# Kernel optimization log

Measured on AMD Instinct MI355X. Metric: run time of the kernel, lower is better.

## Reference

```python
import jax, jax.numpy as jnp
import numpy as np

N_NODES = 50000
N_EDGES = 600000
FEAT = 128
HID = 256


def _sage_gcn(feats, src, dst, W, b, n_nodes):
    # DGL SAGEConv aggregator_type='gcn':
    # h_neigh = (sum_{u in N(v)} h_u + h_v) / (in_deg(v) + 1); out = h_neigh @ W + b
    neigh_sum = jax.ops.segment_sum(feats[src], dst, num_segments=n_nodes)  # [N, d]
    in_deg = jax.ops.segment_sum(jnp.ones((src.shape[0],), feats.dtype), dst,
                                 num_segments=n_nodes)  # [N]
    h = (neigh_sum + feats) / (in_deg + 1.0)[:, None]
    return h @ W + b


def setup_inputs() -> dict:
    key = jax.random.key(0)
    ks = jax.random.split(key, 8)
    s = lambda d: 1.0 / np.sqrt(d)
    return {
        "features": jax.random.normal(ks[0], (N_NODES, FEAT), jnp.float32),
        "src": jax.random.randint(ks[1], (N_EDGES,), 0, N_NODES, jnp.int32),
        "dst": jax.random.randint(ks[2], (N_EDGES,), 0, N_NODES, jnp.int32),
        "W1": jax.random.normal(ks[3], (FEAT, HID), jnp.float32) * s(FEAT),
        "b1": jnp.zeros((HID,), jnp.float32),
        "W2": jax.random.normal(ks[4], (HID, HID), jnp.float32) * s(HID),
        "b2": jnp.zeros((HID,), jnp.float32),
        "Wd1": jax.random.normal(ks[5], (HID, HID), jnp.float32) * s(HID),
        "bd1": jnp.zeros((HID,), jnp.float32),
        "Wd2": jax.random.normal(ks[6], (HID, 1), jnp.float32) * s(HID),
        "bd2": jnp.zeros((1,), jnp.float32),
    }


def reference(features, src, dst, W1, b1, W2, b2, Wd1, bd1, Wd2, bd2):
    n = features.shape[0]
    # Encoder: SAGEConv(gcn) -> ReLU -> SAGEConv(gcn)   (dropout inactive in eval)
    h = _sage_gcn(features, src, dst, W1, b1, n)
    h = jax.nn.relu(h)
    h = _sage_gcn(h, src, dst, W2, b2, n)
    # Decoder: Linear -> ReLU -> Linear
    h = jax.nn.relu(h @ Wd1 + bd1)
    return h @ Wd2 + bd2  # [N, 1]
```

## Files before the change

### kernel.cpp

```cpp
#include <hip/hip_runtime.h>
#include <type_traits>

#define NN 50000
#define NE 600000
#define FEAT 128
#define HID 256
#define MAXD 64

typedef float v4f __attribute__((ext_vector_type(4)));
typedef float f32x4 __attribute__((ext_vector_type(4)));
typedef __bf16 bf16x8 __attribute__((ext_vector_type(8)));
using u16 = unsigned short;
using u32 = unsigned int;
typedef u16 u16x4 __attribute__((ext_vector_type(4)));
typedef u16 u16x8 __attribute__((ext_vector_type(8)));

__device__ __forceinline__ u16 f2bf(float f) {
    u32 u = __builtin_bit_cast(u32, f);
    u += 0x7fffu + ((u >> 16) & 1u);
    return (u16)(u >> 16);
}
__device__ __forceinline__ float bf2f(u16 h) {
    u32 u = ((u32)h) << 16;
    return __builtin_bit_cast(float, u);
}

#define NB_FILL 2344
#define NB_CVT 6250
#define NB_W1  128
#define NB_W2  256
#define NB_WD1 256
__global__ __launch_bounds__(256) void prep_fill_k(const int* __restrict__ src,
                                                   const int* __restrict__ dst,
                                                   int* __restrict__ cnt,
                                                   int* __restrict__ ell,
                                                   const float* __restrict__ feats,
                                                   const float* __restrict__ W1,
                                                   const float* __restrict__ W2,
                                                   const float* __restrict__ Wd1,
                                                   u16* __restrict__ featsbf,
                                                   u16* __restrict__ WT1,
                                                   u16* __restrict__ WT2,
                                                   u16* __restrict__ WTd1) {
    int b = blockIdx.x, t = threadIdx.x;
    if (b < NB_FILL) {
        int e = b * 256 + t;
        if (e < NE) {
            int d = dst[e];
            int p = atomicAdd(&cnt[d], 1);
            if (p < MAXD) ell[(size_t)d * MAXD + p] = src[e];
        }
        return;
    }
    b -= NB_FILL;
    if (b < NB_CVT) {
        int i = b * 256 + t;
        v4f v = *(const v4f*)(feats + (size_t)i * 4);
        u16x4 o;
        #pragma unroll
        for (int j = 0; j < 4; j++) o[j] = f2bf(v[j]);
        *(u16x4*)(featsbf + (size_t)i * 4) = o;
    } else if (b < NB_CVT + NB_W1) {
        int idx = (b - NB_CVT) * 256 + t;
        int k = idx >> 8, n = idx & 255;
        WT1[(size_t)n * 128 + k] = f2bf(W1[idx]);
    } else if (b < NB_CVT + NB_W1 + NB_W2) {
        int idx = (b - NB_CVT - NB_W1) * 256 + t;
        int k = idx >> 8, n = idx & 255;
        WT2[(size_t)n * 256 + k] = f2bf(W2[idx]);
    } else {
        int idx = (b - NB_CVT - NB_W1 - NB_W2) * 256 + t;
        int k = idx >> 8, n = idx & 255;
        WTd1[(size_t)n * 256 + k] = f2bf(Wd1[idx]);
    }
}

template <int D>
__global__ __launch_bounds__(256) void aggregate_bf_k(const u16* __restrict__ x,
                                                      const int* __restrict__ cnt,
                                                      const int* __restrict__ ell,
                                                      u16* __restrict__ o) {
    constexpr int LPG = (D == 256) ? 32 : 16;
    constexpr int G = 64 / LPG;
    int wave = threadIdx.x >> 6;
    int lane = threadIdx.x & 63;
    int v = blockIdx.x * 4 + wave;
    if (v >= NN) return;
    int g  = lane / LPG;
    int li = lane & (LPG - 1);
    size_t coff = (size_t)li * 8;
    int deg = cnt[v]; if (deg > MAXD) deg = MAXD;
    int cntv = deg + 1;
    const int* cols = ell + (size_t)v * MAXD;
    float acc[8];
    #pragma unroll
    for (int i = 0; i < 8; i++) acc[i] = 0.f;
    int base = 0;
    #pragma unroll 4
    for (; base + G <= cntv; base += G) {
        int idx = base + g;
        int row = (idx < deg) ? cols[idx] : v;
        u16x8 r = *(const u16x8*)(x + (size_t)row * D + coff);
        #pragma unroll
        for (int i = 0; i < 8; i++) acc[i] += bf2f(r[i]);
    }
    if (base + g < cntv) {
        int idx = base + g;
        int row = (idx < deg) ? cols[idx] : v;
        u16x8 r = *(const u16x8*)(x + (size_t)row * D + coff);
        #pragma unroll
        for (int i = 0; i < 8; i++) acc[i] += bf2f(r[i]);
    }
    #pragma unroll
    for (int i = 0; i < 8; i++) {
        acc[i] += __shfl_xor(acc[i], 32, 64);
        if (G == 4) acc[i] += __shfl_xor(acc[i], 16, 64);
    }
    if (lane < LPG) {
        float inv = 1.0f / (float)cntv;
        u16x8 O;
        #pragma unroll
        for (int i = 0; i < 8; i++) O[i] = f2bf(acc[i] * inv);
        *(u16x8*)(o + (size_t)v * D + coff) = O;
    }
}

__global__ __launch_bounds__(256) void agg2_dec_k(const u16* __restrict__ x,
                                                  const int* __restrict__ cnt,
                                                  const int* __restrict__ ell,
                                                  const float* __restrict__ bd1,
                                                  const float* __restrict__ wd2,
                                                  const float* __restrict__ bd2,
                                                  float* __restrict__ out) {
    int wave = threadIdx.x >> 6;
    int lane = threadIdx.x & 63;
    int v = blockIdx.x * 4 + wave;
    if (v >= NN) return;
    int g  = lane >> 5;
    int li = lane & 31;
    size_t coff = (size_t)li * 8;
    int deg = cnt[v]; if (deg > MAXD) deg = MAXD;
    int cntv = deg + 1;
    const int* cols = ell + (size_t)v * MAXD;
    float acc[8];
    #pragma unroll
    for (int i = 0; i < 8; i++) acc[i] = 0.f;
    int base = 0;
    #pragma unroll 4
    for (; base + 2 <= cntv; base += 2) {
        int idx = base + g;
        int row = (idx < deg) ? cols[idx] : v;
        u16x8 r = *(const u16x8*)(x + (size_t)row * 256 + coff);
        #pragma unroll
        for (int i = 0; i < 8; i++) acc[i] += bf2f(r[i]);
    }
    if (base + g < cntv) {
        int idx = base + g;
        int row = (idx < deg) ? cols[idx] : v;
        u16x8 r = *(const u16x8*)(x + (size_t)row * 256 + coff);
        #pragma unroll
        for (int i = 0; i < 8; i++) acc[i] += bf2f(r[i]);
    }
    #pragma unroll
    for (int i = 0; i < 8; i++) acc[i] += __shfl_xor(acc[i], 32, 64);

    float inv = 1.0f / (float)cntv;
    v4f b0 = *(const v4f*)(bd1 + li * 8);
    v4f b1 = *(const v4f*)(bd1 + li * 8 + 4);
    v4f w0 = *(const v4f*)(wd2 + li * 8);
    v4f w1 = *(const v4f*)(wd2 + li * 8 + 4);
    float p = 0.f;
    #pragma unroll
    for (int i = 0; i < 4; i++) p += fmaxf(acc[i] * inv + b0[i], 0.f) * w0[i];
    #pragma unroll
    for (int i = 0; i < 4; i++) p += fmaxf(acc[i + 4] * inv + b1[i], 0.f) * w1[i];
    p += __shfl_xor(p, 1, 64);
    p += __shfl_xor(p, 2, 64);
    p += __shfl_xor(p, 4, 64);
    p += __shfl_xor(p, 8, 64);
    p += __shfl_xor(p, 16, 64);
    if (lane == 0) out[v] = p + bd2[0];
}

#define MFMA_BF16 __builtin_amdgcn_mfma_f32_16x16x32_bf16
#define SW(s, r) (((s) ^ (((r) >> 1) & 3)) * 8)

#define MFMA_STEP(pa0, pa1, pa2, pa3, ph0, ph1)              \
    do {                                                     \
        acc[0][0] = MFMA_BF16(pa0, ph0, acc[0][0], 0, 0, 0); \
        acc[0][1] = MFMA_BF16(pa0, ph1, acc[0][1], 0, 0, 0); \
        acc[1][0] = MFMA_BF16(pa1, ph0, acc[1][0], 0, 0, 0); \
        acc[1][1] = MFMA_BF16(pa1, ph1, acc[1][1], 0, 0, 0); \
        acc[2][0] = MFMA_BF16(pa2, ph0, acc[2][0], 0, 0, 0); \
        acc[2][1] = MFMA_BF16(pa2, ph1, acc[2][1], 0, 0, 0); \
        acc[3][0] = MFMA_BF16(pa3, ph0, acc[3][0], 0, 0, 0); \
        acc[3][1] = MFMA_BF16(pa3, ph1, acc[3][1], 0, 0, 0); \
    } while (0)

__global__ __launch_bounds__(512, 4) void fused_gemm123_k(const u16* __restrict__ A1,
                                                          const u16* __restrict__ B1,
                                                          const float* __restrict__ b1,
                                                          const u16* __restrict__ B2,
                                                          const float* __restrict__ b2,
                                                          const u16* __restrict__ B3,
                                                          u16* __restrict__ Z, int M) {
    __shared__ __attribute__((aligned(16))) u16 sA[2][64 * 32];
    __shared__ __attribute__((aligned(16))) u16 sB[2][256 * 32];
    __shared__ __attribute__((aligned(16))) u16 sH[64 * 264];

    int tid = threadIdx.x;
    int wid = tid >> 6, lane = tid & 63;
    int m0 = blockIdx.x * 64;
    int r16 = lane & 15, sl = lane >> 4, k8 = sl * 8;

    u32 ao[4], bo[2];
    #pragma unroll
    for (int mf = 0; mf < 4; mf++) {
        int ar = mf * 16 + r16;
        ao[mf] = ar * 32 + SW(sl, ar);
    }
    #pragma unroll
    for (int nf = 0; nf < 2; nf++) {
        int bc = wid * 32 + nf * 16 + r16;
        bo[nf] = bc * 32 + SW(sl, bc);
    }

    f32x4 acc[4][2];
    #pragma unroll
    for (int a = 0; a < 4; a++)
        #pragma unroll
        for (int b = 0; b < 2; b++) acc[a][b] = (f32x4)0.f;

    int aRow = tid >> 2, aS = tid & 3;
    u32 aSw = aRow * 32 + SW(aS, aRow);
    int gAr = m0 + aRow; if (gAr >= M) gAr = M - 1;
    const u16* gA = A1 + (size_t)gAr * 128 + aS * 8;
    int bRow[2], bS[2]; u32 bSw[2];
    #pragma unroll
    for (int j = 0; j < 2; j++) {
        int idx = tid + j * 512;
        bRow[j] = idx >> 2; bS[j] = idx & 3;
        bSw[j] = bRow[j] * 32 + SW(bS[j], bRow[j]);
    }

    uint4 rA, rB0, rB1;

    if (tid < 256) rA = *(const uint4*)gA;
    rB0 = *(const uint4*)(B1 + (size_t)bRow[0] * 128 + bS[0] * 8);
    rB1 = *(const uint4*)(B1 + (size_t)bRow[1] * 128 + bS[1] * 8);
    if (tid < 256) *(uint4*)(&sA[0][aSw]) = rA;
    *(uint4*)(&sB[0][bSw[0]]) = rB0;
    *(uint4*)(&sB[0][bSw[1]]) = rB1;
    __syncthreads();

    #pragma unroll
    for (int kb = 0; kb < 4; kb++) {
        int cur = kb & 1;
        if (kb < 3) {
            if (tid < 256) rA = *(const uint4*)(gA + (kb + 1) * 32);
            rB0 = *(const uint4*)(B1 + (size_t)bRow[0] * 128 + (kb + 1) * 32 + bS[0] * 8);
            rB1 = *(const uint4*)(B1 + (size_t)bRow[1] * 128 + (kb + 1) * 32 + bS[1] * 8);
        }
        bf16x8 a0 = *(const bf16x8*)(&sA[cur][ao[0]]);
        bf16x8 a1 = *(const bf16x8*)(&sA[cur][ao[1]]);
        bf16x8 a2 = *(const bf16x8*)(&sA[cur][ao[2]]);
        bf16x8 a3 = *(const bf16x8*)(&sA[cur][ao[3]]);
        bf16x8 h0 = *(const bf16x8*)(&sB[cur][bo[0]]);
        bf16x8 h1 = *(const bf16x8*)(&sB[cur][bo[1]]);
        MFMA_STEP(a0, a1, a2, a3, h0, h1);
        if (kb < 3) {
            int nxt = cur ^ 1;
            if (tid < 256) *(uint4*)(&sA[nxt][aSw]) = rA;
            *(uint4*)(&sB[nxt][bSw[0]]) = rB0;
            *(uint4*)(&sB[nxt][bSw[1]]) = rB1;
        }
        __syncthreads();
    }

    rB0 = *(const uint4*)(B2 + (size_t)bRow[0] * 256 + bS[0] * 8);
    rB1 = *(const uint4*)(B2 + (size_t)bRow[1] * 256 + bS[1] * 8);

    {
        float b1c[2];
        #pragma unroll
        for (int nf = 0; nf < 2; nf++) b1c[nf] = b1[wid * 32 + nf * 16 + r16];
        int rbase = sl * 4;
        #pragma unroll
        for (int mf = 0; mf < 4; mf++)
            #pragma unroll
            for (int j = 0; j < 4; j++) {
                int r = mf * 16 + rbase + j;
                #pragma unroll
                for (int nf = 0; nf < 2; nf++) {
                    int c = wid * 32 + nf * 16 + r16;
                    sH[r * 264 + c] = f2bf(fmaxf(acc[mf][nf][j] + b1c[nf], 0.f));
                }
            }
        #pragma unroll
        for (int a = 0; a < 4; a++)
            #pragma unroll
            for (int b = 0; b < 2; b++) acc[a][b] = (f32x4)0.f;
    }
    *(uint4*)(&sB[0][bSw[0]]) = rB0;
    *(uint4*)(&sB[0][bSw[1]]) = rB1;
    __syncthreads();

    #pragma unroll
    for (int kb = 0; kb < 8; kb++) {
        int cur = kb & 1;
        if (kb < 7) {
            rB0 = *(const uint4*)(B2 + (size_t)bRow[0] * 256 + (kb + 1) * 32 + bS[0] * 8);
            rB1 = *(const uint4*)(B2 + (size_t)bRow[1] * 256 + (kb + 1) * 32 + bS[1] * 8);
        }
        bf16x8 a0 = *(const bf16x8*)(sH + (0 * 16 + r16) * 264 + kb * 32 + k8);
        bf16x8 a1 = *(const bf16x8*)(sH + (1 * 16 + r16) * 264 + kb * 32 + k8);
        bf16x8 a2 = *(const bf16x8*)(sH + (2 * 16 + r16) * 264 + kb * 32 + k8);
        bf16x8 a3 = *(const bf16x8*)(sH + (3 * 16 + r16) * 264 + kb * 32 + k8);
        bf16x8 h0 = *(const bf16x8*)(&sB[cur][bo[0]]);
        bf16x8 h1 = *(const bf16x8*)(&sB[cur][bo[1]]);
        MFMA_STEP(a0, a1, a2, a3, h0, h1);
        if (kb < 7) {
            int nxt = cur ^ 1;
            *(uint4*)(&sB[nxt][bSw[0]]) = rB0;
            *(uint4*)(&sB[nxt][bSw[1]]) = rB1;
        }
        __syncthreads();
    }

    rB0 = *(const uint4*)(B3 + (size_t)bRow[0] * 256 + bS[0] * 8);
    rB1 = *(const uint4*)(B3 + (size_t)bRow[1] * 256 + bS[1] * 8);

    {
        float b2c[2];
        #pragma unroll
        for (int nf = 0; nf < 2; nf++) b2c[nf] = b2[wid * 32 + nf * 16 + r16];
        int rbase = sl * 4;
        #pragma unroll
        for (int mf = 0; mf < 4; mf++)
            #pragma unroll
            for (int j = 0; j < 4; j++) {
                int r = mf * 16 + rbase + j;
                #pragma unroll
                for (int nf = 0; nf < 2; nf++) {
                    int c = wid * 32 + nf * 16 + r16;
                    sH[r * 264 + c] = f2bf(acc[mf][nf][j] + b2c[nf]);
                }
            }
        #pragma unroll
        for (int a = 0; a < 4; a++)
            #pragma unroll
            for (int b = 0; b < 2; b++) acc[a][b] = (f32x4)0.f;
    }
    *(uint4*)(&sB[0][bSw[0]]) = rB0;
    *(uint4*)(&sB[0][bSw[1]]) = rB1;
    __syncthreads();

    #pragma unroll
    for (int kb = 0; kb < 8; kb++) {
        int cur = kb & 1;
        if (kb < 7) {
            rB0 = *(const uint4*)(B3 + (size_t)bRow[0] * 256 + (kb + 1) * 32 + bS[0] * 8);
            rB1 = *(const uint4*)(B3 + (size_t)bRow[1] * 256 + (kb + 1) * 32 + bS[1] * 8);
        }
        bf16x8 a0 = *(const bf16x8*)(sH + (0 * 16 + r16) * 264 + kb * 32 + k8);
        bf16x8 a1 = *(const bf16x8*)(sH + (1 * 16 + r16) * 264 + kb * 32 + k8);
        bf16x8 a2 = *(const bf16x8*)(sH + (2 * 16 + r16) * 264 + kb * 32 + k8);
        bf16x8 a3 = *(const bf16x8*)(sH + (3 * 16 + r16) * 264 + kb * 32 + k8);
        bf16x8 h0 = *(const bf16x8*)(&sB[cur][bo[0]]);
        bf16x8 h1 = *(const bf16x8*)(&sB[cur][bo[1]]);
        MFMA_STEP(a0, a1, a2, a3, h0, h1);
        if (kb < 7) {
            int nxt = cur ^ 1;
            *(uint4*)(&sB[nxt][bSw[0]]) = rB0;
            *(uint4*)(&sB[nxt][bSw[1]]) = rB1;
        }
        __syncthreads();
    }

    {
        int rbase = sl * 4;
        #pragma unroll
        for (int mf = 0; mf < 4; mf++)
            #pragma unroll
            for (int j = 0; j < 4; j++) {
                int gr = m0 + mf * 16 + rbase + j;
                if (gr < M) {
                    #pragma unroll
                    for (int nf = 0; nf < 2; nf++) {
                        int gc = wid * 32 + nf * 16 + r16;
                        Z[(size_t)gr * 256 + gc] = f2bf(acc[mf][nf][j]);
                    }
                }
            }
    }
}

extern "C" void kernel_launch(void* const* d_in, const int* in_sizes, int n_in,
                              void* d_out, int out_size, void* d_ws, size_t ws_size,
                              hipStream_t stream) {
    const float* feats = (const float*)d_in[0];
    const int*   src   = (const int*)d_in[1];
    const int*   dst   = (const int*)d_in[2];
    const float* W1    = (const float*)d_in[3];
    const float* b1    = (const float*)d_in[4];
    const float* W2    = (const float*)d_in[5];
    const float* b2    = (const float*)d_in[6];
    const float* Wd1   = (const float*)d_in[7];
    const float* bd1   = (const float*)d_in[8];
    const float* Wd2   = (const float*)d_in[9];
    const float* bd2   = (const float*)d_in[10];
    float* out = (float*)d_out;

    char* base = (char*)d_ws;
    size_t off = 0;
    int* cnt = (int*)(base + off); off += (size_t)NN * 4;
    int* ell = (int*)(base + off); off += (size_t)NN * MAXD * 4;
    u16* WT1  = (u16*)(base + off); off += (size_t)FEAT * 256 * 2;
    u16* WT2  = (u16*)(base + off); off += (size_t)HID * 256 * 2;
    u16* WTd1 = (u16*)(base + off); off += (size_t)HID * 256 * 2;
    off = (off + 255) & ~(size_t)255;
    u16* featsbf = (u16*)(base + off); off += (size_t)NN * FEAT * 2;
    u16* A1      = (u16*)(base + off); off += (size_t)NN * FEAT * 2;
    u16* Zbf     = (u16*)(base + off); off += (size_t)NN * HID * 2;

    hipMemsetAsync(cnt, 0, (size_t)NN * 4, stream);
    prep_fill_k<<<NB_FILL + NB_CVT + NB_W1 + NB_W2 + NB_WD1, 256, 0, stream>>>(
        src, dst, cnt, ell, feats, W1, W2, Wd1, featsbf, WT1, WT2, WTd1);

    aggregate_bf_k<FEAT><<<(NN + 3) / 4, 256, 0, stream>>>(featsbf, cnt, ell, A1);

    fused_gemm123_k<<<(NN + 63) / 64, 512, 0, stream>>>(A1, WT1, b1, WT2, b2, WTd1,
                                                        Zbf, NN);

    agg2_dec_k<<<(NN + 3) / 4, 256, 0, stream>>>(Zbf, cnt, ell, bd1, Wd2, bd2, out);
}
```

Measured before the change: 157.8 us.

## Fold W2 and Wd1 into one precomputed weight matrix to drop a GEMM

Because no nonlinearity sits between the second SAGE linear layer and the first decoder linear layer, W2·Wd1 and b2·Wd1 are precomputed in the prep kernel and the fused GEMM kernel runs two chained matmuls instead of three. This removes one 256x256 GEMM stage per 64-row tile, along with its shared-memory staging and bf16 rounding. In exchange the prep kernel does a small dense 256x256x256 product with naive scalar loops, and the change relies on aggregation commuting with the linear map.

```diff
diff --git a/kernel.cpp b/kernel.cpp
--- a/kernel.cpp
+++ b/kernel.cpp
@@ -28,8 +28,7 @@
 #define NB_FILL 2344
 #define NB_CVT 6250
 #define NB_W1  128
-#define NB_W2  256
-#define NB_WD1 256
+#define NB_W23 256
 __global__ __launch_bounds__(256) void prep_fill_k(const int* __restrict__ src,
                                                    const int* __restrict__ dst,
                                                    int* __restrict__ cnt,
@@ -38,10 +37,11 @@
                                                    const float* __restrict__ W1,
                                                    const float* __restrict__ W2,
                                                    const float* __restrict__ Wd1,
+                                                   const float* __restrict__ b2,
                                                    u16* __restrict__ featsbf,
                                                    u16* __restrict__ WT1,
-                                                   u16* __restrict__ WT2,
-                                                   u16* __restrict__ WTd1) {
+                                                   u16* __restrict__ WT23,
+                                                   float* __restrict__ c23) {
     int b = blockIdx.x, t = threadIdx.x;
     if (b < NB_FILL) {
         int e = b * 256 + t;
@@ -64,14 +64,20 @@
         int idx = (b - NB_CVT) * 256 + t;
         int k = idx >> 8, n = idx & 255;
         WT1[(size_t)n * 128 + k] = f2bf(W1[idx]);
-    } else if (b < NB_CVT + NB_W1 + NB_W2) {
-        int idx = (b - NB_CVT - NB_W1) * 256 + t;
-        int k = idx >> 8, n = idx & 255;
-        WT2[(size_t)n * 256 + k] = f2bf(W2[idx]);
+    } else if (b < NB_CVT + NB_W1 + NB_W23) {
+        int k = b - NB_CVT - NB_W1;
+        int n = t;
+        const float* w2row = W2 + (size_t)k * 256;
+        float acc = 0.f;
+        #pragma unroll 8
+        for (int j = 0; j < 256; j++) acc += w2row[j] * Wd1[(size_t)j * 256 + n];
+        WT23[(size_t)n * 256 + k] = f2bf(acc);
     } else {
-        int idx = (b - NB_CVT - NB_W1 - NB_W2) * 256 + t;
-        int k = idx >> 8, n = idx & 255;
-        WTd1[(size_t)n * 256 + k] = f2bf(Wd1[idx]);
+        int n = t;
+        float acc = 0.f;
+        #pragma unroll 8
+        for (int j = 0; j < 256; j++) acc += b2[j] * Wd1[(size_t)j * 256 + n];
+        c23[n] = acc;
     }
 }
 
@@ -197,13 +203,12 @@
         acc[3][1] = MFMA_BF16(pa3, ph1, acc[3][1], 0, 0, 0); \
     } while (0)
 
-__global__ __launch_bounds__(512, 4) void fused_gemm123_k(const u16* __restrict__ A1,
-                                                          const u16* __restrict__ B1,
-                                                          const float* __restrict__ b1,
-                                                          const u16* __restrict__ B2,
-                                                          const float* __restrict__ b2,
-                                                          const u16* __restrict__ B3,
-                                                          u16* __restrict__ Z, int M) {
+__global__ __launch_bounds__(512, 4) void fused_gemm12_k(const u16* __restrict__ A1,
+                                                         const u16* __restrict__ B1,
+                                                         const float* __restrict__ b1,
+                                                         const u16* __restrict__ B23,
+                                                         const float* __restrict__ c23,
+                                                         u16* __restrict__ Z, int M) {
     __shared__ __attribute__((aligned(16))) u16 sA[2][64 * 32];
     __shared__ __attribute__((aligned(16))) u16 sB[2][256 * 32];
     __shared__ __attribute__((aligned(16))) u16 sH[64 * 264];
@@ -277,8 +282,8 @@
         __syncthreads();
     }
 
-    rB0 = *(const uint4*)(B2 + (size_t)bRow[0] * 256 + bS[0] * 8);
-    rB1 = *(const uint4*)(B2 + (size_t)bRow[1] * 256 + bS[1] * 8);
+    rB0 = *(const uint4*)(B23 + (size_t)bRow[0] * 256 + bS[0] * 8);
+    rB1 = *(const uint4*)(B23 + (size_t)bRow[1] * 256 + bS[1] * 8);
 
     {
         float b1c[2];
@@ -309,8 +314,8 @@
     for (int kb = 0; kb < 8; kb++) {
         int cur = kb & 1;
         if (kb < 7) {
-            rB0 = *(const uint4*)(B2 + (size_t)bRow[0] * 256 + (kb + 1) * 32 + bS[0] * 8);
-            rB1 = *(const uint4*)(B2 + (size_t)bRow[1] * 256 + (kb + 1) * 32 + bS[1] * 8);
+            rB0 = *(const uint4*)(B23 + (size_t)bRow[0] * 256 + (kb + 1) * 32 + bS[0] * 8);
+            rB1 = *(const uint4*)(B23 + (size_t)bRow[1] * 256 + (kb + 1) * 32 + bS[1] * 8);
         }
         bf16x8 a0 = *(const bf16x8*)(sH + (0 * 16 + r16) * 264 + kb * 32 + k8);
         bf16x8 a1 = *(const bf16x8*)(sH + (1 * 16 + r16) * 264 + kb * 32 + k8);
@@ -327,57 +332,10 @@
         __syncthreads();
     }
 
-    rB0 = *(const uint4*)(B3 + (size_t)bRow[0] * 256 + bS[0] * 8);
-    rB1 = *(const uint4*)(B3 + (size_t)bRow[1] * 256 + bS[1] * 8);
-
     {
-        float b2c[2];
-        #pragma unroll
-        for (int nf = 0; nf < 2; nf++) b2c[nf] = b2[wid * 32 + nf * 16 + r16];
-        int rbase = sl * 4;
-        #pragma unroll
-        for (int mf = 0; mf < 4; mf++)
-            #pragma unroll
-            for (int j = 0; j < 4; j++) {
-                int r = mf * 16 + rbase + j;
-                #pragma unroll
-                for (int nf = 0; nf < 2; nf++) {
-                    int c = wid * 32 + nf * 16 + r16;
-                    sH[r * 264 + c] = f2bf(acc[mf][nf][j] + b2c[nf]);
-                }
-            }
-        #pragma unroll
-        for (int a = 0; a < 4; a++)
-            #pragma unroll
-            for (int b = 0; b < 2; b++) acc[a][b] = (f32x4)0.f;
-    }
-    *(uint4*)(&sB[0][bSw[0]]) = rB0;
-    *(uint4*)(&sB[0][bSw[1]]) = rB1;
-    __syncthreads();
-
-    #pragma unroll
-    for (int kb = 0; kb < 8; kb++) {
-        int cur = kb & 1;
-        if (kb < 7) {
-            rB0 = *(const uint4*)(B3 + (size_t)bRow[0] * 256 + (kb + 1) * 32 + bS[0] * 8);
-            rB1 = *(const uint4*)(B3 + (size_t)bRow[1] * 256 + (kb + 1) * 32 + bS[1] * 8);
-        }
-        bf16x8 a0 = *(const bf16x8*)(sH + (0 * 16 + r16) * 264 + kb * 32 + k8);
-        bf16x8 a1 = *(const bf16x8*)(sH + (1 * 16 + r16) * 264 + kb * 32 + k8);
-        bf16x8 a2 = *(const bf16x8*)(sH + (2 * 16 + r16) * 264 + kb * 32 + k8);
-        bf16x8 a3 = *(const bf16x8*)(sH + (3 * 16 + r16) * 264 + kb * 32 + k8);
-        bf16x8 h0 = *(const bf16x8*)(&sB[cur][bo[0]]);
-        bf16x8 h1 = *(const bf16x8*)(&sB[cur][bo[1]]);
-        MFMA_STEP(a0, a1, a2, a3, h0, h1);
-        if (kb < 7) {
-            int nxt = cur ^ 1;
-            *(uint4*)(&sB[nxt][bSw[0]]) = rB0;
-            *(uint4*)(&sB[nxt][bSw[1]]) = rB1;
-        }
-        __syncthreads();
-    }
-
-    {
+        float cc[2];
+        #pragma unroll
+        for (int nf = 0; nf < 2; nf++) cc[nf] = c23[wid * 32 + nf * 16 + r16];
         int rbase = sl * 4;
         #pragma unroll
         for (int mf = 0; mf < 4; mf++)
@@ -388,7 +346,7 @@
                     #pragma unroll
                     for (int nf = 0; nf < 2; nf++) {
                         int gc = wid * 32 + nf * 16 + r16;
-                        Z[(size_t)gr * 256 + gc] = f2bf(acc[mf][nf][j]);
+                        Z[(size_t)gr * 256 + gc] = f2bf(acc[mf][nf][j] + cc[nf]);
                     }
                 }
             }
@@ -415,22 +373,22 @@
     size_t off = 0;
     int* cnt = (int*)(base + off); off += (size_t)NN * 4;
     int* ell = (int*)(base + off); off += (size_t)NN * MAXD * 4;
-    u16* WT1  = (u16*)(base + off); off += (size_t)FEAT * 256 * 2;
-    u16* WT2  = (u16*)(base + off); off += (size_t)HID * 256 * 2;
-    u16* WTd1 = (u16*)(base + off); off += (size_t)HID * 256 * 2;
+    u16* WT1   = (u16*)(base + off); off += (size_t)FEAT * 256 * 2;
+    u16* WT23  = (u16*)(base + off); off += (size_t)HID * 256 * 2;
+    float* c23 = (float*)(base + off); off += 256 * 4;
     off = (off + 255) & ~(size_t)255;
     u16* featsbf = (u16*)(base + off); off += (size_t)NN * FEAT * 2;
     u16* A1      = (u16*)(base + off); off += (size_t)NN * FEAT * 2;
     u16* Zbf     = (u16*)(base + off); off += (size_t)NN * HID * 2;
 
     hipMemsetAsync(cnt, 0, (size_t)NN * 4, stream);
-    prep_fill_k<<<NB_FILL + NB_CVT + NB_W1 + NB_W2 + NB_WD1, 256, 0, stream>>>(
-        src, dst, cnt, ell, feats, W1, W2, Wd1, featsbf, WT1, WT2, WTd1);
+    prep_fill_k<<<NB_FILL + NB_CVT + NB_W1 + NB_W23 + 1, 256, 0, stream>>>(
+        src, dst, cnt, ell, feats, W1, W2, Wd1, b2, featsbf, WT1, WT23, c23);
 
     aggregate_bf_k<FEAT><<<(NN + 3) / 4, 256, 0, stream>>>(featsbf, cnt, ell, A1);
 
-    fused_gemm123_k<<<(NN + 63) / 64, 512, 0, stream>>>(A1, WT1, b1, WT2, b2, WTd1,
-                                                        Zbf, NN);
+    fused_gemm12_k<<<(NN + 63) / 64, 512, 0, stream>>>(A1, WT1, b1, WT23, c23,
+                                                       Zbf, NN);
 
     agg2_dec_k<<<(NN + 3) / 4, 256, 0, stream>>>(Zbf, cnt, ell, bd1, Wd2, bd2, out);
 }
```

Measured after the change: 157.4 us. About the same (-0.2%).
